# Performance work log

Hardware: AMD Instinct MI355X
Metric: run time of the kernel (lower is better)

Reference implementation:

```python
import jax, jax.numpy as jnp
import numpy as np

B, S, D = 1, 2048, 1024
H = 16            # num_heads
DH = D // H       # head dim = 64
WIN = 128         # local window size
DIL = 4           # dilation rate


def setup_inputs() -> dict:
    key = jax.random.key(0)
    k1, k2, k3 = jax.random.split(key, 3)
    x = jax.random.normal(k1, (B, S, D), jnp.float32)
    w_qkv = jax.random.normal(k2, (D, 3 * D), jnp.float32) * 0.02
    w_out = jax.random.normal(k3, (D, D), jnp.float32) * 0.02
    return {"x": x, "w_qkv": w_qkv, "w_out": w_out}


def reference(x, w_qkv, w_out):
    b, s, d = x.shape
    scale = 1.0 / np.sqrt(DH).astype(np.float32)

    qkv = x @ w_qkv                                   # [B,S,3D]
    q, k, v = jnp.split(qkv, 3, axis=-1)
    q = q.reshape(b, s, H, DH)
    k = k.reshape(b, s, H, DH)
    v = v.reshape(b, s, H, DH)

    # ---- local window attention: attend within non-overlapping windows ----
    nw = s // WIN
    qw = q.reshape(b, nw, WIN, H, DH)
    kw = k.reshape(b, nw, WIN, H, DH)
    vw = v.reshape(b, nw, WIN, H, DH)
    s_loc = jnp.einsum('bnihd,bnjhd->bnhij', qw, kw) * scale
    p_loc = jax.nn.softmax(s_loc, axis=-1)
    o_loc = jnp.einsum('bnhij,bnjhd->bnihd', p_loc, vw).reshape(b, s, H, DH)

    # ---- dilated attention: attend within each stride-DIL residue class ----
    n = s // DIL
    # seq index = i*DIL + g  -> position i within dilation group g
    qd = q.reshape(b, n, DIL, H, DH)
    kd = k.reshape(b, n, DIL, H, DH)
    vd = v.reshape(b, n, DIL, H, DH)
    s_dil = jnp.einsum('bighd,bjghd->bghij', qd, kd) * scale
    p_dil = jax.nn.softmax(s_dil, axis=-1)
    o_dil = jnp.einsum('bghij,bjghd->bighd', p_dil, vd).reshape(b, s, H, DH)

    # ---- global full attention ----
    s_glb = jnp.einsum('bihd,bjhd->bhij', q, k) * scale
    p_glb = jax.nn.softmax(s_glb, axis=-1)
    o_glb = jnp.einsum('bhij,bjhd->bihd', p_glb, v)

    # fuse the three scales (uniform average) and project out
    o = (o_loc + o_dil + o_glb) * (1.0 / 3.0)
    return o.reshape(b, s, d) @ w_out
```

## Files before the change

### kernel.cpp

```cpp
#include <hip/hip_runtime.h>
#include <hip/hip_bf16.h>


typedef __attribute__((ext_vector_type(8))) short s8v;
typedef __attribute__((ext_vector_type(4))) float f4v;

#define QSCALE 0.18033688011112042f

__device__ __forceinline__ short f2bf(float f) {
  union { float f; unsigned u; } x; x.f = f;
  unsigned r = (x.u + 0x7FFF + ((x.u >> 16) & 1)) >> 16;
  return (short)r;
}
__device__ __forceinline__ f4v mfma16(s8v a, s8v b, f4v c) {
  return __builtin_amdgcn_mfma_f32_16x16x32_bf16(a, b, c, 0, 0, 0);
}
__device__ __forceinline__ void load_lds16(const void* g, void* l) {
  __builtin_amdgcn_global_load_lds(
      (const __attribute__((address_space(1))) unsigned int*)g,
      (__attribute__((address_space(3))) unsigned int*)l, 16, 0, 0);
}
__device__ __forceinline__ float exp2f_fast(float x) {
  return __builtin_amdgcn_exp2f(x);
}
__device__ __forceinline__ unsigned cvt_pk_bf16(float lo, float hi) {
  unsigned r;
  asm("v_cvt_pk_bf16_f32 %0, %1, %2" : "=v"(r) : "v"(lo), "v"(hi));
  return r;
}

__global__ __launch_bounds__(256)
void fill_const_kernel(float* __restrict__ out, int n, float v) {
  int i = blockIdx.x * 256 + threadIdx.x;
  if (i < n) out[i] = v;
}

__global__ __launch_bounds__(256)
void prep_fused(const float* __restrict__ wq, short* __restrict__ wqT,
                const float* __restrict__ wo, short* __restrict__ woT,
                const float* __restrict__ x, short* __restrict__ xb) {
  const int bx = blockIdx.x, t = threadIdx.x;
  __shared__ float T[64][69];
  if (bx >= 64) {
    if (x) {
      int cb = (bx - 64) * 16 + blockIdx.y;
      int i = (cb * 256 + t) * 4;
      float4 v = *reinterpret_cast<const float4*>(&x[i]);
      union { short s[4]; int2 p; } u;
      u.s[0] = f2bf(v.x); u.s[1] = f2bf(v.y); u.s[2] = f2bf(v.z); u.s[3] = f2bf(v.w);
      *reinterpret_cast<int2*>(&xb[i]) = u.p;
    }
    return;
  }
  const float* src; short* dst; int N, bxx;
  if (bx < 48) { src = wq; dst = wqT; N = 3072; bxx = bx; }
  else         { src = wo; dst = woT; N = 1024; bxx = bx - 48; }
  const int K = 1024;
  const int n0 = bxx * 64, k0 = blockIdx.y * 64;
  for (int jb = t; jb < 1024; jb += 256) {
    int r = jb >> 4, c4 = (jb & 15) * 4;
    float4 v = *reinterpret_cast<const float4*>(&src[(size_t)(k0 + r) * N + n0 + c4]);
    T[c4 + 0][r] = v.x; T[c4 + 1][r] = v.y; T[c4 + 2][r] = v.z; T[c4 + 3][r] = v.w;
  }
  __syncthreads();
  for (int jb = t; jb < 512; jb += 256) {
    int n = jb >> 3, k8 = (jb & 7) * 8;
    union { short s[8]; int4 v; } p;
#pragma unroll
    for (int i = 0; i < 8; ++i) p.s[i] = f2bf(T[n][k8 + i]);
    *reinterpret_cast<int4*>(&dst[(size_t)(n0 + n) * K + k0 + k8]) = p.v;
  }
}

__device__ __forceinline__ void g1_epilogue_store(
    int gcol, int grow0, const f4v& a,
    short* __restrict__ qb, short* __restrict__ kb, short* __restrict__ vT) {
  if (gcol >= 2048) {
    int d = gcol - 2048;
    int j = grow0 >> 2;
    int gb = ((j >> 6) << 6) + (((j >> 5) & 1) << 5) +
             (((j >> 2) & 3) << 3) + (((j >> 4) & 1) << 2) + (j & 3);
    size_t base = (size_t)d * 2048 + gb;
#pragma unroll
    for (int r = 0; r < 4; ++r)
      vT[base + (r << 9)] = f2bf(a[r]);
  } else {
    short* dst = (gcol < 1024) ? qb : kb;
    float sc = (gcol < 1024) ? QSCALE : 1.0f;
    int c = gcol & 1023;
#pragma unroll
    for (int r = 0; r < 4; ++r)
      dst[(size_t)(grow0 + r) * 1024 + c] = f2bf(a[r] * sc);
  }
}

template <int COUT, bool AF32, int NT, int KH>
__global__ __launch_bounds__(256)
void gemm_tile(const void* __restrict__ Av, const short* __restrict__ Bt,
               short* __restrict__ qb, short* __restrict__ kb,
               short* __restrict__ vT, float* __restrict__ co,
               int K, int N) {
  __shared__ __align__(16) short As[KH][64 * 32];
  __shared__ __align__(16) short Bs[KH][NT * 32];
  const int tid = threadIdx.x, wave = tid >> 6;
  const int li = tid & 63;
  const int row0 = blockIdx.y * 64, col0 = blockIdx.x * NT;
  const int lr = li & 15, quad = li >> 4, lk = quad * 8;
  constexpr int NTW = NT / 64;

  f4v acc[4][NTW];
#pragma unroll
  for (int i = 0; i < 4; ++i)
#pragma unroll
    for (int j = 0; j < NTW; ++j) acc[i][j] = (f4v){0.f, 0.f, 0.f, 0.f};

  for (int k0 = 0; k0 < K; k0 += 32 * KH) {
    __syncthreads();
#pragma unroll
    for (int kk = 0; kk < KH; ++kk) {
#pragma unroll
      for (int u = 0; u < NTW; ++u)
        load_lds16(Bt + (size_t)(col0 + u * 64 + (tid >> 2)) * K + k0 + kk * 32 + (tid & 3) * 8,
                   &Bs[kk][u * 2048 + wave * 512]);
      if (AF32) {
        const float* A = (const float*)Av;
#pragma unroll
        for (int c = 0; c < 2; ++c) {
          int j = c * 256 + tid;
          int r = j >> 3, c4 = (j & 7) * 4;
          float4 v = *reinterpret_cast<const float4*>(
              &A[(size_t)(row0 + r) * K + k0 + kk * 32 + c4]);
          union { short s[4]; int2 v2; } p;
          p.s[0] = f2bf(v.x); p.s[1] = f2bf(v.y); p.s[2] = f2bf(v.z); p.s[3] = f2bf(v.w);
          *reinterpret_cast<int2*>(&As[kk][r * 32 + c4]) = p.v2;
        }
      } else {
        load_lds16((const short*)Av + (size_t)(row0 + (tid >> 2)) * K + k0 + kk * 32 + (tid & 3) * 8,
                   &As[kk][wave * 512]);
      }
    }
    __syncthreads();

#pragma unroll
    for (int kk = 0; kk < KH; ++kk) {
      s8v af[4], bfr[NTW];
#pragma unroll
      for (int mt = 0; mt < 4; ++mt)
        af[mt] = *reinterpret_cast<const s8v*>(&As[kk][(mt * 16 + lr) * 32 + lk]);
#pragma unroll
      for (int u = 0; u < NTW; ++u)
        bfr[u] = *reinterpret_cast<const s8v*>(&Bs[kk][(wave * (NT / 4) + u * 16 + lr) * 32 + lk]);
#pragma unroll
      for (int mt = 0; mt < 4; ++mt)
#pragma unroll
        for (int u = 0; u < NTW; ++u)
          acc[mt][u] = mfma16(af[mt], bfr[u], acc[mt][u]);
    }
  }

#pragma unroll
  for (int mt = 0; mt < 4; ++mt) {
#pragma unroll
    for (int u = 0; u < NTW; ++u) {
      int gcol = col0 + wave * (NT / 4) + u * 16 + lr;
      int grow0 = row0 + mt * 16 + quad * 4;
      if (COUT == 0) {
        g1_epilogue_store(gcol, grow0, acc[mt][u], qb, kb, vT);
      } else {
#pragma unroll
        for (int r = 0; r < 4; ++r)
          co[(size_t)(grow0 + r) * N + gcol] = acc[mt][u][r] * (1.0f / 3.0f);
      }
    }
  }
}

__global__ __launch_bounds__(512, 2)
void attn_unified(const short* __restrict__ qb, const short* __restrict__ kb,
                  const short* __restrict__ vT, short* __restrict__ o) {
  __shared__ __align__(16) short Ks[4][64][72];
  __shared__ __align__(16) short Vt[4][64][72];
  __shared__ float lX[2][4][16][4];

  const int tid = threadIdx.x;
  const int wave = tid >> 6, li = tid & 63;
  const int grp = wave >> 2, wr = wave & 3;
  const int b = blockIdx.x, h = b & 15, g = b >> 4;
  const int qcol = h * 64;
  const int lr = li & 15, quad = li >> 4, lk = quad * 8;
  const int wt2 = g >> 2;
  const int wH  = (g >> 1) & 1;
  const bool wgrp = (grp == wH);
  const int sr = tid >> 3, sc8 = (tid & 7) * 8;

  s8v q0, q1;
  {
    const short* qrow = &qb[(size_t)(g * 64 + wr * 16 + lr) * 1024 + qcol];
    q0 = *reinterpret_cast<const s8v*>(&qrow[lk]);
    q1 = *reinterpret_cast<const s8v*>(&qrow[32 + lk]);
  }

#pragma unroll
  for (int c = 0; c < 2; ++c) {
    int ks = (c * 64 + sr) << 2;
    *reinterpret_cast<int4*>(&Ks[c][sr][sc8]) =
        *reinterpret_cast<const int4*>(&kb[(size_t)ks * 1024 + qcol + sc8]);
    *reinterpret_cast<int4*>(&Vt[c][sr][sc8]) =
        *reinterpret_cast<const int4*>(&vT[(size_t)(h * 64 + sr) * 2048 + c * 64 + sc8]);
  }
  __syncthreads();

  float l_r = 0.f, l_loc = 0.f, l_dil = 0.f;
  f4v oacc[4], o_loc[4], o_dil[4];
#pragma unroll
  for (int i = 0; i < 4; ++i) {
    oacc[i]  = (f4v){0.f, 0.f, 0.f, 0.f};
    o_loc[i] = (f4v){0.f, 0.f, 0.f, 0.f};
    o_dil[i] = (f4v){0.f, 0.f, 0.f, 0.f};
  }

  const int koffA = ((grp * 2 + 0) * 16 + lr) * 72 + lk;
  const int koffB = ((grp * 2 + 1) * 16 + lr) * 72 + lk;
  const int voff  = lr * 72 + grp * 32 + lk;
  const short* KsF = &Ks[0][0][0];
  const short* VtF = &Vt[0][0][0];

#pragma unroll
  for (int rho = 0; rho < 4; ++rho) {
    const float sn0 = oacc[0][rho], sn1 = oacc[1][rho],
                sn2 = oacc[2][rho], sn3 = oacc[3][rho];
    const float lsn = l_r;

#pragma unroll 2
    for (int p8 = 0; p8 < 4; ++p8) {
      const int tA = rho * 8 + 2 * p8;
      const int bufA = (2 * p8) & 3;
      const int cbA = bufA * 4608, cbB = cbA + 4608;
      const bool pf = (tA < 30);
      const bool wtA = wgrp && (2 * p8 == wt2);
      const bool wtB = wgrp && (2 * p8 + 1 == wt2);

      int4 kpA, vpA, kpB, vpB;
      if (pf) {
        const int tnA = tA + 2, tnB = tA + 3;
        const int ksA = ((((tnA & 7) << 6) + sr) << 2) + (tnA >> 3);
        const int ksB = ((((tnB & 7) << 6) + sr) << 2) + (tnB >> 3);
        kpA = *reinterpret_cast<const int4*>(&kb[(size_t)ksA * 1024 + qcol + sc8]);
        vpA = *reinterpret_cast<const int4*>(
            &vT[(size_t)(h * 64 + sr) * 2048 + tnA * 64 + sc8]);
        kpB = *reinterpret_cast<const int4*>(&kb[(size_t)ksB * 1024 + qcol + sc8]);
        vpB = *reinterpret_cast<const int4*>(
            &vT[(size_t)(h * 64 + sr) * 2048 + tnB * 64 + sc8]);
      }

      {
        f4v s4a = (f4v){0.f, 0.f, 0.f, 0.f};
        f4v s4b = (f4v){0.f, 0.f, 0.f, 0.f};
        s4a = mfma16(*reinterpret_cast<const s8v*>(&KsF[cbA + koffA]), q0, s4a);
        s4b = mfma16(*reinterpret_cast<const s8v*>(&KsF[cbA + koffB]), q0, s4b);
        s4a = mfma16(*reinterpret_cast<const s8v*>(&KsF[cbA + koffA + 32]), q1, s4a);
        s4b = mfma16(*reinterpret_cast<const s8v*>(&KsF[cbA + koffB + 32]), q1, s4b);

        float pa0 = exp2f_fast(s4a[0]), pa1 = exp2f_fast(s4a[1]),
              pa2 = exp2f_fast(s4a[2]), pa3 = exp2f_fast(s4a[3]);
        float pb0 = exp2f_fast(s4b[0]), pb1 = exp2f_fast(s4b[1]),
              pb2 = exp2f_fast(s4b[2]), pb3 = exp2f_fast(s4b[3]);
        float ps = ((pa0 + pa1) + (pa2 + pa3)) + ((pb0 + pb1) + (pb2 + pb3));
        union { unsigned u[4]; s8v v; } pk;
        pk.u[0] = cvt_pk_bf16(pa0, pa1);
        pk.u[1] = cvt_pk_bf16(pa2, pa3);
        pk.u[2] = cvt_pk_bf16(pb0, pb1);
        pk.u[3] = cvt_pk_bf16(pb2, pb3);
        l_r += ps;
        if (wtA) l_loc += ps;

        if (wtA) {
#pragma unroll
          for (int nt = 0; nt < 4; ++nt) {
            s8v bv = *reinterpret_cast<const s8v*>(&VtF[cbA + nt * 1152 + voff]);
            f4v dd = mfma16(pk.v, bv, (f4v){0.f, 0.f, 0.f, 0.f});
            oacc[nt] += dd;
            o_loc[nt] += dd;
          }
        } else {
#pragma unroll
          for (int nt = 0; nt < 4; ++nt) {
            s8v bv = *reinterpret_cast<const s8v*>(&VtF[cbA + nt * 1152 + voff]);
            oacc[nt] = mfma16(pk.v, bv, oacc[nt]);
          }
        }
      }

      {
        f4v s4a = (f4v){0.f, 0.f, 0.f, 0.f};
        f4v s4b = (f4v){0.f, 0.f, 0.f, 0.f};
        s4a = mfma16(*reinterpret_cast<const s8v*>(&KsF[cbB + koffA]), q0, s4a);
        s4b = mfma16(*reinterpret_cast<const s8v*>(&KsF[cbB + koffB]), q0, s4b);
        s4a = mfma16(*reinterpret_cast<const s8v*>(&KsF[cbB + koffA + 32]), q1, s4a);
        s4b = mfma16(*reinterpret_cast<const s8v*>(&KsF[cbB + koffB + 32]), q1, s4b);

        float pa0 = exp2f_fast(s4a[0]), pa1 = exp2f_fast(s4a[1]),
              pa2 = exp2f_fast(s4a[2]), pa3 = exp2f_fast(s4a[3]);
        float pb0 = exp2f_fast(s4b[0]), pb1 = exp2f_fast(s4b[1]),
              pb2 = exp2f_fast(s4b[2]), pb3 = exp2f_fast(s4b[3]);
        float ps = ((pa0 + pa1) + (pa2 + pa3)) + ((pb0 + pb1) + (pb2 + pb3));
        union { unsigned u[4]; s8v v; } pk;
        pk.u[0] = cvt_pk_bf16(pa0, pa1);
        pk.u[1] = cvt_pk_bf16(pa2, pa3);
        pk.u[2] = cvt_pk_bf16(pb0, pb1);
        pk.u[3] = cvt_pk_bf16(pb2, pb3);
        l_r += ps;
        if (wtB) l_loc += ps;

        if (wtB) {
#pragma unroll
          for (int nt = 0; nt < 4; ++nt) {
            s8v bv = *reinterpret_cast<const s8v*>(&VtF[cbB + nt * 1152 + voff]);
            f4v dd = mfma16(pk.v, bv, (f4v){0.f, 0.f, 0.f, 0.f});
            oacc[nt] += dd;
            o_loc[nt] += dd;
          }
        } else {
#pragma unroll
          for (int nt = 0; nt < 4; ++nt) {
            s8v bv = *reinterpret_cast<const s8v*>(&VtF[cbB + nt * 1152 + voff]);
            oacc[nt] = mfma16(pk.v, bv, oacc[nt]);
          }
        }
      }

      if (pf) {
        const int wbA = bufA ^ 2;
        *reinterpret_cast<int4*>(&Ks[wbA][sr][sc8])     = kpA;
        *reinterpret_cast<int4*>(&Vt[wbA][sr][sc8])     = vpA;
        *reinterpret_cast<int4*>(&Ks[wbA + 1][sr][sc8]) = kpB;
        *reinterpret_cast<int4*>(&Vt[wbA + 1][sr][sc8]) = vpB;
      }
      __syncthreads();
    }

    if (((lr ^ rho) & 3) == 0) l_dil = l_r - lsn;
    o_dil[0][rho] = oacc[0][rho] - sn0;
    o_dil[1][rho] = oacc[1][rho] - sn1;
    o_dil[2][rho] = oacc[2][rho] - sn2;
    o_dil[3][rho] = oacc[3][rho] - sn3;
  }

  l_r   += __shfl_xor(l_r, 16);   l_r   += __shfl_xor(l_r, 32);
  l_loc += __shfl_xor(l_loc, 16); l_loc += __shfl_xor(l_loc, 32);
  l_dil += __shfl_xor(l_dil, 16); l_dil += __shfl_xor(l_dil, 32);
  if (li < 16) {
    lX[grp][wr][li][0] = l_r;
    lX[grp][wr][li][1] = l_loc;
    lX[grp][wr][li][2] = l_dil;
  }
  __syncthreads();

  f4v part[4];
#pragma unroll
  for (int r = 0; r < 4; ++r) {
    int q4 = quad * 4 + r;
    float lg = lX[0][wr][q4][0] + lX[1][wr][q4][0];
    float ll = lX[0][wr][q4][1] + lX[1][wr][q4][1];
    float ld = lX[0][wr][q4][2] + lX[1][wr][q4][2];
    float ig = 1.0f / lg, il = 1.0f / ll, id = 1.0f / ld;
#pragma unroll
    for (int nt = 0; nt < 4; ++nt)
      part[nt][r] = oacc[nt][r] * ig + o_loc[nt][r] * il + o_dil[nt][r] * id;
  }

  float* xch = reinterpret_cast<float*>(&Ks[0][0][0]);
  const int slot = wr * 64 + li;
  if (grp == 1) {
#pragma unroll
    for (int nt = 0; nt < 4; ++nt)
#pragma unroll
      for (int hh = 0; hh < 2; ++hh) {
        float2 v2 = make_float2(part[nt][2 * hh], part[nt][2 * hh + 1]);
        *reinterpret_cast<float2*>(&xch[slot * 18 + (nt * 2 + hh) * 2]) = v2;
      }
  }
  __syncthreads();
  if (grp == 0) {
#pragma unroll
    for (int nt = 0; nt < 4; ++nt)
#pragma unroll
      for (int hh = 0; hh < 2; ++hh) {
        float2 v2 = *reinterpret_cast<const float2*>(&xch[slot * 18 + (nt * 2 + hh) * 2]);
        part[nt][2 * hh]     += v2.x;
        part[nt][2 * hh + 1] += v2.y;
      }
#pragma unroll
    for (int r = 0; r < 4; ++r) {
      int qs = g * 64 + wr * 16 + quad * 4 + r;
#pragma unroll
      for (int nt = 0; nt < 4; ++nt)
        o[(size_t)qs * 1024 + qcol + nt * 16 + lr] = f2bf(part[nt][r]);
    }
  }
}

extern "C" void kernel_launch(void* const* d_in, const int* in_sizes, int n_in,
                              void* d_out, int out_size, void* d_ws, size_t ws_size,
                              hipStream_t stream) {
  float* out = (float*)d_out;
  const int nfill = (out_size + 255) / 256;
  if (n_in != 3) { fill_const_kernel<<<nfill, 256, 0, stream>>>(out, out_size, 0.5f); return; }
  int ix = -1, iq = -1, io = -1;
  for (int i = 0; i < 3; ++i) {
    if      (in_sizes[i] == 2097152) ix = i;
    else if (in_sizes[i] == 3145728) iq = i;
    else if (in_sizes[i] == 1048576) io = i;
  }
  if (ix < 0 || iq < 0 || io < 0) { fill_const_kernel<<<nfill, 256, 0, stream>>>(out, out_size, 0.3f); return; }
  const float* x     = (const float*)d_in[ix];
  const float* w_qkv = (const float*)d_in[iq];
  const float* w_out = (const float*)d_in[io];

  char* ws = (char*)d_ws;
  const size_t MB = 1048576;
  const size_t needX = 24 * MB;
  const size_t needY = 20 * MB;

  if (ws_size >= needX) {
    short* qb     = (short*)(ws);
    short* kb     = (short*)(ws + 4 * MB);
    short* vT     = (short*)(ws + 8 * MB);
    short* w_qkvT = (short*)(ws + 12 * MB);
    short* o      = (short*)(ws + 12 * MB);
    short* w_outT = (short*)(ws + 18 * MB);
    short* xb     = (short*)(ws + 20 * MB);
    prep_fused<<<dim3(192, 16), 256, 0, stream>>>(w_qkv, w_qkvT, w_out, w_outT, x, xb);
    gemm_tile<0, false, 128, 4><<<dim3(24, 32), 256, 0, stream>>>(xb, w_qkvT, qb, kb, vT, nullptr, 1024, 3072);
    attn_unified<<<512, 512, 0, stream>>>(qb, kb, vT, o);
    gemm_tile<1, false, 64, 2><<<dim3(16, 32), 256, 0, stream>>>(o, w_outT, nullptr, nullptr, nullptr, out, 1024, 1024);
  } else if (ws_size >= needY) {
    short* w_outT = (short*)(ws);
    short* qb     = (short*)(ws + 2 * MB);
    short* kb     = (short*)(ws + 6 * MB);
    short* vT     = (short*)(ws + 10 * MB);
    short* w_qkvT = (short*)(ws + 14 * MB);
    short* o      = (short*)(ws + 14 * MB);
    prep_fused<<<dim3(64, 16), 256, 0, stream>>>(w_qkv, w_qkvT, w_out, w_outT, nullptr, nullptr);
    gemm_tile<0, true, 128, 4><<<dim3(24, 32), 256, 0, stream>>>(x, w_qkvT, qb, kb, vT, nullptr, 1024, 3072);
    attn_unified<<<512, 512, 0, stream>>>(qb, kb, vT, o);
    gemm_tile<1, false, 64, 2><<<dim3(16, 32), 256, 0, stream>>>(o, w_outT, nullptr, nullptr, nullptr, out, 1024, 1024);
  } else {
    fill_const_kernel<<<nfill, 256, 0, stream>>>(out, out_size, 0.2f);
  }
}
```

Baseline: 148.2 us.

## Use direct global-to-LDS loads with XOR-swizzled K/V tiles in attention

```diff
diff --git a/kernel.cpp b/kernel.cpp
--- a/kernel.cpp
+++ b/kernel.cpp
@@ -178,8 +178,8 @@
 __global__ __launch_bounds__(512, 2)
 void attn_unified(const short* __restrict__ qb, const short* __restrict__ kb,
                   const short* __restrict__ vT, short* __restrict__ o) {
-  __shared__ __align__(16) short Ks[4][64][72];
-  __shared__ __align__(16) short Vt[4][64][72];
+  __shared__ __align__(16) short Ks[4][64][64];
+  __shared__ __align__(16) short Vt[4][64][64];
   __shared__ float lX[2][4][16][4];
 
   const int tid = threadIdx.x;
@@ -191,7 +191,13 @@
   const int wt2 = g >> 2;
   const int wH  = (g >> 1) & 1;
   const bool wgrp = (grp == wH);
-  const int sr = tid >> 3, sc8 = (tid & 7) * 8;
+
+  const int srow = tid >> 3, spc = tid & 7;
+  const int sq8 = spc ^ (srow & 7);
+  short* KsB = &Ks[0][0][0];
+  short* VtB = &Vt[0][0][0];
+  short* ldsKW = KsB + wave * 512;
+  short* ldsVW = VtB + wave * 512;
 
   s8v q0, q1;
   {
@@ -202,11 +208,10 @@
 
 #pragma unroll
   for (int c = 0; c < 2; ++c) {
-    int ks = (c * 64 + sr) << 2;
-    *reinterpret_cast<int4*>(&Ks[c][sr][sc8]) =
-        *reinterpret_cast<const int4*>(&kb[(size_t)ks * 1024 + qcol + sc8]);
-    *reinterpret_cast<int4*>(&Vt[c][sr][sc8]) =
-        *reinterpret_cast<const int4*>(&vT[(size_t)(h * 64 + sr) * 2048 + c * 64 + sc8]);
+    const int ksr = (c * 64 + srow) << 2;
+    load_lds16(&kb[(size_t)ksr * 1024 + qcol + sq8 * 8], ldsKW + c * 4096);
+    load_lds16(&vT[(size_t)(h * 64 + srow) * 2048 + c * 64 + sq8 * 8],
+               ldsVW + c * 4096);
   }
   __syncthreads();
 
@@ -219,11 +224,13 @@
     o_dil[i] = (f4v){0.f, 0.f, 0.f, 0.f};
   }
 
-  const int koffA = ((grp * 2 + 0) * 16 + lr) * 72 + lk;
-  const int koffB = ((grp * 2 + 1) * 16 + lr) * 72 + lk;
-  const int voff  = lr * 72 + grp * 32 + lk;
-  const short* KsF = &Ks[0][0][0];
-  const short* VtF = &Vt[0][0][0];
+  const int xa = lr & 7;
+  const int rowA = (grp * 32 + lr) * 64, rowB = rowA + 16 * 64;
+  const int kco0 = ((quad ^ xa) << 3);
+  const int kco1 = (((4 + quad) ^ xa) << 3);
+  const int vco  = ((((grp << 2) + quad) ^ xa) << 3);
+  const short* KsF = KsB;
+  const short* VtF = VtB;
 
 #pragma unroll
   for (int rho = 0; rho < 4; ++rho) {
@@ -235,31 +242,32 @@
     for (int p8 = 0; p8 < 4; ++p8) {
       const int tA = rho * 8 + 2 * p8;
       const int bufA = (2 * p8) & 3;
-      const int cbA = bufA * 4608, cbB = cbA + 4608;
+      const int cbA = bufA * 4096, cbB = cbA + 4096;
       const bool pf = (tA < 30);
       const bool wtA = wgrp && (2 * p8 == wt2);
       const bool wtB = wgrp && (2 * p8 + 1 == wt2);
 
-      int4 kpA, vpA, kpB, vpB;
       if (pf) {
+        const int wb = bufA ^ 2;
         const int tnA = tA + 2, tnB = tA + 3;
-        const int ksA = ((((tnA & 7) << 6) + sr) << 2) + (tnA >> 3);
-        const int ksB = ((((tnB & 7) << 6) + sr) << 2) + (tnB >> 3);
-        kpA = *reinterpret_cast<const int4*>(&kb[(size_t)ksA * 1024 + qcol + sc8]);
-        vpA = *reinterpret_cast<const int4*>(
-            &vT[(size_t)(h * 64 + sr) * 2048 + tnA * 64 + sc8]);
-        kpB = *reinterpret_cast<const int4*>(&kb[(size_t)ksB * 1024 + qcol + sc8]);
-        vpB = *reinterpret_cast<const int4*>(
-            &vT[(size_t)(h * 64 + sr) * 2048 + tnB * 64 + sc8]);
+        const int krA = ((((tnA & 7) << 6) + srow) << 2) + (tnA >> 3);
+        const int krB = ((((tnB & 7) << 6) + srow) << 2) + (tnB >> 3);
+        load_lds16(&kb[(size_t)krA * 1024 + qcol + sq8 * 8], ldsKW + wb * 4096);
+        load_lds16(&vT[(size_t)(h * 64 + srow) * 2048 + tnA * 64 + sq8 * 8],
+                   ldsVW + wb * 4096);
+        load_lds16(&kb[(size_t)krB * 1024 + qcol + sq8 * 8],
+                   ldsKW + (wb + 1) * 4096);
+        load_lds16(&vT[(size_t)(h * 64 + srow) * 2048 + tnB * 64 + sq8 * 8],
+                   ldsVW + (wb + 1) * 4096);
       }
 
       {
         f4v s4a = (f4v){0.f, 0.f, 0.f, 0.f};
         f4v s4b = (f4v){0.f, 0.f, 0.f, 0.f};
-        s4a = mfma16(*reinterpret_cast<const s8v*>(&KsF[cbA + koffA]), q0, s4a);
-        s4b = mfma16(*reinterpret_cast<const s8v*>(&KsF[cbA + koffB]), q0, s4b);
-        s4a = mfma16(*reinterpret_cast<const s8v*>(&KsF[cbA + koffA + 32]), q1, s4a);
-        s4b = mfma16(*reinterpret_cast<const s8v*>(&KsF[cbA + koffB + 32]), q1, s4b);
+        s4a = mfma16(*reinterpret_cast<const s8v*>(&KsF[cbA + rowA + kco0]), q0, s4a);
+        s4b = mfma16(*reinterpret_cast<const s8v*>(&KsF[cbA + rowB + kco0]), q0, s4b);
+        s4a = mfma16(*reinterpret_cast<const s8v*>(&KsF[cbA + rowA + kco1]), q1, s4a);
+        s4b = mfma16(*reinterpret_cast<const s8v*>(&KsF[cbA + rowB + kco1]), q1, s4b);
 
         float pa0 = exp2f_fast(s4a[0]), pa1 = exp2f_fast(s4a[1]),
               pa2 = exp2f_fast(s4a[2]), pa3 = exp2f_fast(s4a[3]);
@@ -277,7 +285,8 @@
         if (wtA) {
 #pragma unroll
           for (int nt = 0; nt < 4; ++nt) {
-            s8v bv = *reinterpret_cast<const s8v*>(&VtF[cbA + nt * 1152 + voff]);
+            s8v bv = *reinterpret_cast<const s8v*>(
+                &VtF[cbA + (nt * 16 + lr) * 64 + vco]);
             f4v dd = mfma16(pk.v, bv, (f4v){0.f, 0.f, 0.f, 0.f});
             oacc[nt] += dd;
             o_loc[nt] += dd;
@@ -285,7 +294,8 @@
         } else {
 #pragma unroll
           for (int nt = 0; nt < 4; ++nt) {
-            s8v bv = *reinterpret_cast<const s8v*>(&VtF[cbA + nt * 1152 + voff]);
+            s8v bv = *reinterpret_cast<const s8v*>(
+                &VtF[cbA + (nt * 16 + lr) * 64 + vco]);
             oacc[nt] = mfma16(pk.v, bv, oacc[nt]);
           }
         }
@@ -294,10 +304,10 @@
       {
         f4v s4a = (f4v){0.f, 0.f, 0.f, 0.f};
         f4v s4b = (f4v){0.f, 0.f, 0.f, 0.f};
-        s4a = mfma16(*reinterpret_cast<const s8v*>(&KsF[cbB + koffA]), q0, s4a);
-        s4b = mfma16(*reinterpret_cast<const s8v*>(&KsF[cbB + koffB]), q0, s4b);
-        s4a = mfma16(*reinterpret_cast<const s8v*>(&KsF[cbB + koffA + 32]), q1, s4a);
-        s4b = mfma16(*reinterpret_cast<const s8v*>(&KsF[cbB + koffB + 32]), q1, s4b);
+        s4a = mfma16(*reinterpret_cast<const s8v*>(&KsF[cbB + rowA + kco0]), q0, s4a);
+        s4b = mfma16(*reinterpret_cast<const s8v*>(&KsF[cbB + rowB + kco0]), q0, s4b);
+        s4a = mfma16(*reinterpret_cast<const s8v*>(&KsF[cbB + rowA + kco1]), q1, s4a);
+        s4b = mfma16(*reinterpret_cast<const s8v*>(&KsF[cbB + rowB + kco1]), q1, s4b);
 
         float pa0 = exp2f_fast(s4a[0]), pa1 = exp2f_fast(s4a[1]),
               pa2 = exp2f_fast(s4a[2]), pa3 = exp2f_fast(s4a[3]);
@@ -315,7 +325,8 @@
         if (wtB) {
 #pragma unroll
           for (int nt = 0; nt < 4; ++nt) {
-            s8v bv = *reinterpret_cast<const s8v*>(&VtF[cbB + nt * 1152 + voff]);
+            s8v bv = *reinterpret_cast<const s8v*>(
+                &VtF[cbB + (nt * 16 + lr) * 64 + vco]);
             f4v dd = mfma16(pk.v, bv, (f4v){0.f, 0.f, 0.f, 0.f});
             oacc[nt] += dd;
             o_loc[nt] += dd;
@@ -323,19 +334,13 @@
         } else {
 #pragma unroll
           for (int nt = 0; nt < 4; ++nt) {
-            s8v bv = *reinterpret_cast<const s8v*>(&VtF[cbB + nt * 1152 + voff]);
+            s8v bv = *reinterpret_cast<const s8v*>(
+                &VtF[cbB + (nt * 16 + lr) * 64 + vco]);
             oacc[nt] = mfma16(pk.v, bv, oacc[nt]);
           }
         }
       }
 
-      if (pf) {
-        const int wbA = bufA ^ 2;
-        *reinterpret_cast<int4*>(&Ks[wbA][sr][sc8])     = kpA;
-        *reinterpret_cast<int4*>(&Vt[wbA][sr][sc8])     = vpA;
-        *reinterpret_cast<int4*>(&Ks[wbA + 1][sr][sc8]) = kpB;
-        *reinterpret_cast<int4*>(&Vt[wbA + 1][sr][sc8]) = vpB;
-      }
       __syncthreads();
     }
 
@@ -431,7 +436,7 @@
     short* w_outT = (short*)(ws + 18 * MB);
     short* xb     = (short*)(ws + 20 * MB);
     prep_fused<<<dim3(192, 16), 256, 0, stream>>>(w_qkv, w_qkvT, w_out, w_outT, x, xb);
-    gemm_tile<0, false, 128, 4><<<dim3(24, 32), 256, 0, stream>>>(xb, w_qkvT, qb, kb, vT, nullptr, 1024, 3072);
+    gemm_tile<0, false, 128, 2><<<dim3(24, 32), 256, 0, stream>>>(xb, w_qkvT, qb, kb, vT, nullptr, 1024, 3072);
     attn_unified<<<512, 512, 0, stream>>>(qb, kb, vT, o);
     gemm_tile<1, false, 64, 2><<<dim3(16, 32), 256, 0, stream>>>(o, w_outT, nullptr, nullptr, nullptr, out, 1024, 1024);
   } else if (ws_size >= needY) {
@@ -442,7 +447,7 @@
     short* w_qkvT = (short*)(ws + 14 * MB);
     short* o      = (short*)(ws + 14 * MB);
     prep_fused<<<dim3(64, 16), 256, 0, stream>>>(w_qkv, w_qkvT, w_out, w_outT, nullptr, nullptr);
-    gemm_tile<0, true, 128, 4><<<dim3(24, 32), 256, 0, stream>>>(x, w_qkvT, qb, kb, vT, nullptr, 1024, 3072);
+    gemm_tile<0, true, 128, 2><<<dim3(24, 32), 256, 0, stream>>>(x, w_qkvT, qb, kb, vT, nullptr, 1024, 3072);
     attn_unified<<<512, 512, 0, stream>>>(qb, kb, vT, o);
     gemm_tile<1, false, 64, 2><<<dim3(16, 32), 256, 0, stream>>>(o, w_outT, nullptr, nullptr, nullptr, out, 1024, 1024);
   } else {
```

After: 143.3 us, median of 2. 1.03x faster.
